# Performance work log

Measured on AMD Instinct MI355X. Metric: run time of the kernel, lower is better.

Reference implementation:

```python
import jax, jax.numpy as jnp
import numpy as np

N_POS = 1024
ALPHA = 0.3
B, S = 32, 1024


def setup_inputs() -> dict:
    key = jax.random.key(0)
    k1, k2, k3, k4 = jax.random.split(key, 4)
    s_arc = jax.random.normal(k1, (B, S, S), dtype=jnp.float32)
    a_arc = jax.random.normal(k2, (B, S, S), dtype=jnp.float32)
    adds = jax.random.randint(k3, (B, S), 0, N_POS, dtype=jnp.int32)
    pos = jax.random.randint(k4, (B, S), 0, N_POS, dtype=jnp.int32)
    return {"s_arc": s_arc, "a_arc": a_arc, "adds": adds, "pos": pos}


def reference(s_arc, a_arc, adds, pos):
    n_bins = N_POS * N_POS
    # --- histogram (scatter-add) of a_arc by POS-pair index ---
    # original: _add[b,p1,p2] = adds[b,p1]*seq_len + adds[b,p2]
    sl = adds.shape[1]
    pair_idx = adds[:, :, None] * sl + adds[:, None, :]            # [B,S,S]
    # indices >= n_bins never match any bin in the original masked-sum loop;
    # segment_sum with num_segments=n_bins drops them identically.
    hist = jax.ops.segment_sum(a_arc.reshape(-1), pair_idx.reshape(-1),
                               num_segments=n_bins)                # [n_pos^2]
    score_arc = jax.nn.sigmoid(hist)
    # --- gather score back into s_arc ---
    slp = pos.shape[1]
    pidx = pos[:, :, None] * slp + pos[:, None, :]                  # [B,S,S]
    valid = pidx < n_bins
    gathered = score_arc[jnp.clip(pidx, 0, n_bins - 1)]
    return s_arc + ALPHA * jnp.where(valid, gathered, jnp.float32(0))
```

## Files before the change

kernel.cpp:

```cpp
#include <hip/hip_runtime.h>

#define NPOS 1024
#define BB   32
#define SS   1024
#define ALPHA_C 0.3f
#define CAP  128
#define PAD  1024
#define OCAP 1024
#define MAXO 16
#define PADPAIR 0x04000400u

__global__ __launch_bounds__(256) void zero_fill(float4* __restrict__ p) {
    p[blockIdx.x * 256 + threadIdx.x] = make_float4(0.f, 0.f, 0.f, 0.f);
}

__global__ __launch_bounds__(256) void build_rowlists(
    const int* __restrict__ adds, int* __restrict__ cnt, int* __restrict__ list) {
    const int i = blockIdx.x * 256 + threadIdx.x;
    const int r = adds[i];
    const int slot = atomicAdd(&cnt[r], 1);
    if (slot < CAP) list[r * CAP + slot] = i;
}

__global__ __launch_bounds__(1024) void build_colell(
    const int* __restrict__ adds, ushort* __restrict__ ell16,
    int* __restrict__ ocnt, int* __restrict__ oent) {
    __shared__ int scnt[NPOS];
    __shared__ int so;
    const int b = blockIdx.x, t = threadIdx.x;
    const int c = adds[b * SS + t];
    ((uint2*)ell16)[b * 1024 + t] = make_uint2(PADPAIR, PADPAIR);
    scnt[t] = 0;
    if (t == 0) so = 0;
    __syncthreads();
    const int slot = atomicAdd(&scnt[c], 1);
    if (slot < 4) {
        ell16[(((size_t)b * 512 + (c & 511)) * 2 + (c >> 9)) * 4 + slot] = (ushort)t;
    } else {
        const int o = atomicAdd(&so, 1);
        if (o < OCAP) oent[b * OCAP + o] = (c << 10) | t;
    }
    __syncthreads();
    if (t == 0) ocnt[b] = (so < OCAP) ? so : OCAP;
}

__global__ __launch_bounds__(256) void overflow_fixup(
    const float* __restrict__ a, const int* __restrict__ adds,
    const int* __restrict__ ocnt, const int* __restrict__ oent,
    float* __restrict__ hist) {
    const int b  = blockIdx.x;
    const int ei = blockIdx.y;
    if (ei >= ocnt[b]) return;
    const int e  = oent[b * OCAP + ei];
    const int c  = e >> 10, p2 = e & 1023;
    const int p1 = blockIdx.z * 256 + threadIdx.x;
    const int r  = adds[b * SS + p1];
    const float v = a[((size_t)(b * SS + p1)) * SS + p2];
    atomicAdd(&hist[(size_t)r * NPOS + c], v);
}

__global__ __launch_bounds__(512) void hist_rows_kernel(
    const float* __restrict__ a, const int* __restrict__ rowcnt,
    const int* __restrict__ rowlist, const ushort* __restrict__ ell16,
    float* __restrict__ hist) {
    __shared__ float buf[2][NPOS + 2];
    __shared__ int   lsrc[CAP];
    const int r = blockIdx.x, t = threadIdx.x;

    int n = rowcnt[r]; if (n > CAP) n = CAP;
    if (t < CAP && t < n) lsrc[t] = rowlist[r * CAP + t];
    if (t == 0) { buf[0][PAD] = 0.f; buf[1][PAD] = 0.f; }
    __syncthreads();

    const uint4* ellv = (const uint4*)ell16;
    float acc0 = 0.f, acc1 = 0.f;
    uint4  E = make_uint4(PADPAIR, PADPAIR, PADPAIR, PADPAIR);
    float2 Rb = make_float2(0.f, 0.f);

    if (n > 0) {
        const int s0 = lsrc[0];
        const float2 R0 = ((const float2*)(a + (size_t)s0 * SS))[t];
        E = ellv[(size_t)(s0 >> 10) * 512 + t];
        ((float2*)buf[0])[t] = R0;
    }
    if (n > 1) {
        const int s1 = lsrc[1];
        Rb = ((const float2*)(a + (size_t)s1 * SS))[t];
    }
    __syncthreads();

    for (int k = 0; k < n; ++k) {
        uint4 F = make_uint4(PADPAIR, PADPAIR, PADPAIR, PADPAIR);
        if (k + 1 < n) F = ellv[(size_t)(lsrc[k + 1] >> 10) * 512 + t];

        const float* rb = buf[k & 1];
        acc0 += rb[E.x & 0xffffu]; acc0 += rb[E.x >> 16];
        acc0 += rb[E.y & 0xffffu]; acc0 += rb[E.y >> 16];
        acc1 += rb[E.z & 0xffffu]; acc1 += rb[E.z >> 16];
        acc1 += rb[E.w & 0xffffu]; acc1 += rb[E.w >> 16];
        __builtin_amdgcn_sched_barrier(0);

        if (k + 1 < n) ((float2*)buf[(k + 1) & 1])[t] = Rb;
        if (k + 2 < n) Rb = ((const float2*)(a + (size_t)lsrc[k + 2] * SS))[t];

        E = F;
        asm volatile("s_waitcnt lgkmcnt(0)" ::: "memory");
        __builtin_amdgcn_s_barrier();
    }

    const size_t o0 = (size_t)r * NPOS + t;
    const float base0 = hist[o0], base1 = hist[o0 + 512];
    hist[o0]       = 1.f / (1.f + __expf(-(base0 + acc0)));
    hist[o0 + 512] = 1.f / (1.f + __expf(-(base1 + acc1)));
}

__global__ __launch_bounds__(256) void gather_kernel(
    const float* __restrict__ s, const int* __restrict__ pos,
    const float* __restrict__ score, float* __restrict__ out) {
    const int row = blockIdx.x;
    const int b   = row >> 10;
    const int*  posb = pos + b * SS;
    const int   base = posb[row & 1023] * NPOS;
    const size_t off = (size_t)row * SS;

    const int t = threadIdx.x;
    float4 v = ((const float4*)(s + off))[t];
    int4   c = ((const int4*)posb)[t];
    float4 o;
    o.x = v.x + ALPHA_C * score[base + c.x];
    o.y = v.y + ALPHA_C * score[base + c.y];
    o.z = v.z + ALPHA_C * score[base + c.z];
    o.w = v.w + ALPHA_C * score[base + c.w];
    ((float4*)(out + off))[t] = o;
}

extern "C" void kernel_launch(void* const* d_in, const int* in_sizes, int n_in,
                              void* d_out, int out_size, void* d_ws, size_t ws_size,
                              hipStream_t stream) {
    const float* s_arc = (const float*)d_in[0];
    const float* a_arc = (const float*)d_in[1];
    const int*   adds  = (const int*)d_in[2];
    const int*   pos   = (const int*)d_in[3];
    float* out  = (float*)d_out;

    float*  hist  = (float*)d_ws;
    int*    cnt   = (int*)((char*)d_ws + (size_t)NPOS * NPOS * sizeof(float));
    int*    list  = cnt + NPOS;
    ushort* ell16 = (ushort*)(list + NPOS * CAP);
    int*    ocnt  = (int*)(ell16 + (size_t)BB * NPOS * 4);
    int*    oent  = ocnt + BB;

    zero_fill<<<1025, 256, 0, stream>>>((float4*)hist);
    build_rowlists<<<(BB * SS) / 256, 256, 0, stream>>>(adds, cnt, list);
    build_colell<<<BB, 1024, 0, stream>>>(adds, ell16, ocnt, oent);
    overflow_fixup<<<dim3(BB, MAXO, SS / 256), 256, 0, stream>>>(a_arc, adds, ocnt, oent, hist);
    hist_rows_kernel<<<NPOS, 512, 0, stream>>>(a_arc, cnt, list, ell16, hist);
    gather_kernel<<<BB * SS, 256, 0, stream>>>(s_arc, pos, hist, out);
}
```

Measured before the change: 141.2 us.

## Fuse table-building kernels and load rows directly into LDS via global_load_lds

Merges the row-list and column-ELL builder kernels into one launch, removing a kernel launch and a separate pass over adds. In the histogram kernel, row data is now copied from global memory straight into the LDS double buffer with global_load_lds, bypassing registers. The old two-deep register prefetch becomes a one-deep prefetch followed by a vmcnt wait every iteration, which may expose more memory latency.

Result: no change. 138.6 us (-1.8%).

```diff
diff --git a/kernel.cpp b/kernel.cpp
--- a/kernel.cpp
+++ b/kernel.cpp
@@ -10,21 +10,16 @@
 #define MAXO 16
 #define PADPAIR 0x04000400u
 
+typedef const __attribute__((address_space(1))) unsigned int guint;
+typedef __attribute__((address_space(3))) unsigned int luint;
+
 __global__ __launch_bounds__(256) void zero_fill(float4* __restrict__ p) {
     p[blockIdx.x * 256 + threadIdx.x] = make_float4(0.f, 0.f, 0.f, 0.f);
 }
 
-__global__ __launch_bounds__(256) void build_rowlists(
-    const int* __restrict__ adds, int* __restrict__ cnt, int* __restrict__ list) {
-    const int i = blockIdx.x * 256 + threadIdx.x;
-    const int r = adds[i];
-    const int slot = atomicAdd(&cnt[r], 1);
-    if (slot < CAP) list[r * CAP + slot] = i;
-}
-
-__global__ __launch_bounds__(1024) void build_colell(
-    const int* __restrict__ adds, ushort* __restrict__ ell16,
-    int* __restrict__ ocnt, int* __restrict__ oent) {
+__global__ __launch_bounds__(1024) void build_tables(
+    const int* __restrict__ adds, int* __restrict__ cnt, int* __restrict__ list,
+    ushort* __restrict__ ell16, int* __restrict__ ocnt, int* __restrict__ oent) {
     __shared__ int scnt[NPOS];
     __shared__ int so;
     const int b = blockIdx.x, t = threadIdx.x;
@@ -33,6 +28,8 @@
     scnt[t] = 0;
     if (t == 0) so = 0;
     __syncthreads();
+    const int rslot = atomicAdd(&cnt[c], 1);
+    if (rslot < CAP) list[c * CAP + rslot] = b * SS + t;
     const int slot = atomicAdd(&scnt[c], 1);
     if (slot < 4) {
         ell16[(((size_t)b * 512 + (c & 511)) * 2 + (c >> 9)) * 4 + slot] = (ushort)t;
@@ -66,6 +63,7 @@
     __shared__ float buf[2][NPOS + 2];
     __shared__ int   lsrc[CAP];
     const int r = blockIdx.x, t = threadIdx.x;
+    const int w = t >> 6, lane = t & 63;
 
     int n = rowcnt[r]; if (n > CAP) n = CAP;
     if (t < CAP && t < n) lsrc[t] = rowlist[r * CAP + t];
@@ -74,22 +72,25 @@
 
     const uint4* ellv = (const uint4*)ell16;
     float acc0 = 0.f, acc1 = 0.f;
-    uint4  E = make_uint4(PADPAIR, PADPAIR, PADPAIR, PADPAIR);
-    float2 Rb = make_float2(0.f, 0.f);
+    uint4 E = make_uint4(PADPAIR, PADPAIR, PADPAIR, PADPAIR);
 
     if (n > 0) {
-        const int s0 = lsrc[0];
-        const float2 R0 = ((const float2*)(a + (size_t)s0 * SS))[t];
-        E = ellv[(size_t)(s0 >> 10) * 512 + t];
-        ((float2*)buf[0])[t] = R0;
-    }
-    if (n > 1) {
-        const int s1 = lsrc[1];
-        Rb = ((const float2*)(a + (size_t)s1 * SS))[t];
+        if (w < 4) {
+            guint* gp = (guint*)(a + (size_t)lsrc[0] * SS + (w << 8) + (lane << 2));
+            luint* lp = (luint*)(void*)&buf[0][w << 8];
+            __builtin_amdgcn_global_load_lds(gp, lp, 16, 0, 0);
+        }
+        E = ellv[(size_t)(lsrc[0] >> 10) * 512 + t];
+        asm volatile("s_waitcnt vmcnt(0)" ::: "memory");
     }
     __syncthreads();
 
     for (int k = 0; k < n; ++k) {
+        if (k + 1 < n && w < 4) {
+            guint* gp = (guint*)(a + (size_t)lsrc[k + 1] * SS + (w << 8) + (lane << 2));
+            luint* lp = (luint*)(void*)&buf[(k + 1) & 1][w << 8];
+            __builtin_amdgcn_global_load_lds(gp, lp, 16, 0, 0);
+        }
         uint4 F = make_uint4(PADPAIR, PADPAIR, PADPAIR, PADPAIR);
         if (k + 1 < n) F = ellv[(size_t)(lsrc[k + 1] >> 10) * 512 + t];
 
@@ -98,13 +99,9 @@
         acc0 += rb[E.y & 0xffffu]; acc0 += rb[E.y >> 16];
         acc1 += rb[E.z & 0xffffu]; acc1 += rb[E.z >> 16];
         acc1 += rb[E.w & 0xffffu]; acc1 += rb[E.w >> 16];
-        __builtin_amdgcn_sched_barrier(0);
+        E = F;
 
-        if (k + 1 < n) ((float2*)buf[(k + 1) & 1])[t] = Rb;
-        if (k + 2 < n) Rb = ((const float2*)(a + (size_t)lsrc[k + 2] * SS))[t];
-
-        E = F;
-        asm volatile("s_waitcnt lgkmcnt(0)" ::: "memory");
+        asm volatile("s_waitcnt vmcnt(0) lgkmcnt(0)" ::: "memory");
         __builtin_amdgcn_s_barrier();
     }
 
@@ -151,8 +148,7 @@
     int*    oent  = ocnt + BB;
 
     zero_fill<<<1025, 256, 0, stream>>>((float4*)hist);
-    build_rowlists<<<(BB * SS) / 256, 256, 0, stream>>>(adds, cnt, list);
-    build_colell<<<BB, 1024, 0, stream>>>(adds, ell16, ocnt, oent);
+    build_tables<<<BB, 1024, 0, stream>>>(adds, cnt, list, ell16, ocnt, oent);
     overflow_fixup<<<dim3(BB, MAXO, SS / 256), 256, 0, stream>>>(a_arc, adds, ocnt, oent, hist);
     hist_rows_kernel<<<NPOS, 512, 0, stream>>>(a_arc, cnt, list, ell16, hist);
     gather_kernel<<<BB * SS, 256, 0, stream>>>(s_arc, pos, hist, out);
```
